# Performance work log

Measured on AMD Instinct MI355X. Metric: run time of the kernel, lower is better.

Reference implementation:

```python
import jax, jax.numpy as jnp
import numpy as np

B, S, D = 32, 1024, 256
F_, K = 256, 3
T = 8192
LN_EPS = 1e-5


def _conv1d(x, w, b, padding):
    # x: [B, S, C_in], w: [C_out, C_in, K] -> [B, S, C_out]
    y = jax.lax.conv_general_dilated(
        x.transpose(0, 2, 1), w, window_strides=(1,),
        padding=[(padding, padding)], dimension_numbers=('NCH', 'OIH', 'NCH'))
    return y.transpose(0, 2, 1) + b


def _layernorm(x, g, b):
    mu = jnp.mean(x, axis=-1, keepdims=True)
    var = jnp.mean(jnp.square(x - mu), axis=-1, keepdims=True)
    return (x - mu) * jax.lax.rsqrt(var + LN_EPS) * g + b


def setup_inputs() -> dict:
    key = jax.random.key(0)
    ks = jax.random.split(key, 8)
    sc = 0.02
    return {
        'x': jax.random.normal(ks[0], (B, S, D), dtype=jnp.float32),
        'mask': jnp.zeros((B, S), dtype=bool),
        'duration': jax.random.randint(ks[1], (B, S), 0, 8, dtype=jnp.int32),
        'max_len': T,
        'conv1_w': jax.random.normal(ks[2], (F_, D, K), dtype=jnp.float32) * sc,
        'conv1_b': jnp.zeros((F_,), dtype=jnp.float32),
        'ln1_g': jnp.ones((F_,), dtype=jnp.float32),
        'ln1_b': jnp.zeros((F_,), dtype=jnp.float32),
        'conv2_w': jax.random.normal(ks[3], (F_, F_, K), dtype=jnp.float32) * sc,
        'conv2_b': jnp.zeros((F_,), dtype=jnp.float32),
        'ln2_g': jnp.ones((F_,), dtype=jnp.float32),
        'ln2_b': jnp.zeros((F_,), dtype=jnp.float32),
        'lin_w': jax.random.normal(ks[4], (F_, 1), dtype=jnp.float32) * sc,
        'lin_b': jnp.zeros((1,), dtype=jnp.float32),
    }


def reference(x, mask, duration, max_len, conv1_w, conv1_b, ln1_g, ln1_b,
              conv2_w, conv2_b, ln2_g, ln2_b, lin_w, lin_b):
    # ---- duration predictor (eval mode: dropout = identity) ----
    h = _conv1d(x, conv1_w, conv1_b, (K - 1) // 2)
    h = _layernorm(jax.nn.relu(h), ln1_g, ln1_b)
    h = _conv1d(h, conv2_w, conv2_b, 1)
    h = _layernorm(jax.nn.relu(h), ln2_g, ln2_b)
    log_dur = (h @ lin_w + lin_b)[..., 0]  # [B, S]
    log_dur = jnp.where(mask, 0.0, log_dur)

    # ---- length regulator: repeat_interleave + pad, done as one gather ----
    dur = duration.astype(jnp.int32)
    cum = jnp.cumsum(dur, axis=1)                                   # [B, S]
    t = jnp.arange(max_len, dtype=jnp.int32)                        # [T]
    src_idx = jax.vmap(lambda c: jnp.searchsorted(c, t, side='right'))(cum)  # [B, T]
    mel_len = jnp.minimum(cum[:, -1], max_len)                      # [B]
    valid = t[None, :] < mel_len[:, None]                           # [B, T]
    src_idx = jnp.clip(src_idx, 0, x.shape[1] - 1)
    out = jnp.take_along_axis(x, src_idx[:, :, None], axis=1)       # [B, T, D]
    out = jnp.where(valid[:, :, None], out, 0.0)
    # duration_target path -> duration_rounded = duration, mel_mask stays None
    return out, log_dur, dur, mel_len
```

## Files before the change

kernel.cpp:

```cpp
#include <hip/hip_runtime.h>
#include <cstddef>

constexpr int Bb   = 32;
constexpr int Ss   = 1024;
constexpr int Dd   = 256;
constexpr int Ff   = 256;
constexpr int TMAX = 8192;
constexpr int MM   = Bb * Ss;
constexpr int KK   = 768;
constexpr int SP   = 1026;
constexpr float LN_EPS = 1e-5f;
constexpr int OPIT = 264;

constexpr int GEMM_BLK  = MM / 64;
constexpr int RIDER_PER = 2048;
constexpr int RIDER_F4  = 4096;

constexpr int PREP_W   = 1536;
constexpr int PREP_X   = Bb * SP * 64 / 256;
constexpr int PREP_CUM = Bb;
constexpr int PREP_PAD = 16;
constexpr int PREP_TOT = PREP_W + PREP_X + PREP_CUM + PREP_PAD;

typedef __bf16 bf16x8 __attribute__((ext_vector_type(8)));
typedef __bf16 bf16x4 __attribute__((ext_vector_type(4)));
typedef float  f32x4  __attribute__((ext_vector_type(4)));

#define GLOAD_LDS16(gp, lp)                                                     \
    __builtin_amdgcn_global_load_lds(                                           \
        (const __attribute__((address_space(1))) void*)(gp),                    \
        (__attribute__((address_space(3))) void*)(lp), 16, 0, 0)

__global__ __launch_bounds__(256) void prep_k(
    const float* __restrict__ w1, const float* __restrict__ w2,
    __bf16* __restrict__ wTTs1, __bf16* __restrict__ wTTs2,
    const float* __restrict__ x, __bf16* __restrict__ xp1,
    const int* __restrict__ dur, float* __restrict__ dur_out,
    float* __restrict__ mel_out, int* __restrict__ idx,
    __bf16* __restrict__ xp2)
{
    __shared__ int ic[1024];
    __shared__ int sc[256];
    const int blk = blockIdx.x;
    const int tid = threadIdx.x;

    if (blk < PREP_W) {
        int i = blk * 256 + tid;
        const float* w = w1;
        __bf16* o = wTTs1;
        int j = i;
        if (j >= Ff * KK) { j -= Ff * KK; w = w2; o = wTTs2; }
        int e   = j & 7;
        int cph = (j >> 3) & 7;
        int r   = (j >> 6) & 255;
        int st  = j >> 14;
        int clog = cph ^ (r & 7);
        int kk  = st * 64 + clog * 8 + e;
        int k   = kk >> 8, d = kk & 255;
        o[j] = (__bf16)w[((size_t)(r * 256 + d)) * 3 + k];
        return;
    }
    if (blk < PREP_W + PREP_X) {
        int i   = (blk - PREP_W) * 256 + tid;
        int row = i >> 6;
        int d4  = (i & 63) * 4;
        int b   = row / SP;
        int j   = row - b * SP;
        bf16x4 o = (bf16x4)(__bf16)0.f;
        if (j != 0 && j != SP - 1) {
            float4 v = *(const float4*)&x[(((size_t)(b << 10) + (j - 1)) << 8) + d4];
            o[0] = (__bf16)v.x; o[1] = (__bf16)v.y;
            o[2] = (__bf16)v.z; o[3] = (__bf16)v.w;
        }
        *(bf16x4*)&xp1[((size_t)row << 8) + d4] = o;
        return;
    }
    if (blk >= PREP_W + PREP_X + PREP_CUM) {
        int j = (blk - (PREP_W + PREP_X + PREP_CUM)) * 256 + tid;
        int b = j >> 7;
        int r = (j >> 6) & 1;
        int d = (j & 63) * 4;
        *(bf16x4*)&xp2[((size_t)b * SP + (size_t)r * (SP - 1)) * 256 + d] =
            (bf16x4)(__bf16)0.f;
        return;
    }
    int b = blk - (PREP_W + PREP_X);
    int4 d4 = ((const int4*)(dur + b * 1024))[tid];
    int l0 = d4.x, l1 = l0 + d4.y, l2 = l1 + d4.z, l3 = l2 + d4.w;
    sc[tid] = l3;
    __syncthreads();
    for (int off = 1; off < 256; off <<= 1) {
        int v = (tid >= off) ? sc[tid - off] : 0;
        __syncthreads();
        sc[tid] += v;
        __syncthreads();
    }
    int excl = sc[tid] - l3;
    ((int4*)ic)[tid] = make_int4(excl + l0, excl + l1, excl + l2, excl + l3);
    ((float4*)(dur_out + b * 1024))[tid] =
        make_float4((float)d4.x, (float)d4.y, (float)d4.z, (float)d4.w);
    if (tid == 255) mel_out[b] = (float)min(excl + l3, TMAX);
    __syncthreads();
    int mel = min(ic[1023], TMAX);
    for (int t = tid; t < TMAX; t += 256) {
        int lo = 0, hi = 1024;
        #pragma unroll
        for (int it = 0; it < 10; ++it) {
            int mid = (lo + hi) >> 1;
            if (ic[mid] <= t) lo = mid + 1; else hi = mid;
        }
        idx[b * TMAX + t] = (t < mel) ? min(lo, 1023) : -1;
    }
}

template<int MODE>
__global__ __launch_bounds__(256, 3) void gemm_fused(
    const float* __restrict__ Xf,
    const __bf16* __restrict__ Ap,
    const __bf16* __restrict__ BwS,
    const float* __restrict__ bias,
    const float* __restrict__ g, const float* __restrict__ bt,
    const float* __restrict__ lw, const float* __restrict__ lb,
    const unsigned char* __restrict__ mask,
    __bf16* __restrict__ outB, float* __restrict__ outF,
    const int* __restrict__ idx, f32x4* __restrict__ outv)
{
    __shared__ __bf16 SMEM[64 * 64 + 256 * 64 + 1088];
    __bf16* As = SMEM;
    __bf16* Bs = SMEM + 4096;

    const int tid = threadIdx.x;

    if (blockIdx.x >= GEMM_BLK) {
        int rblk = blockIdx.x - GEMM_BLK + MODE * RIDER_PER;
        size_t base = (size_t)rblk * RIDER_F4 + tid;
        int sarr[16];
        #pragma unroll
        for (int it = 0; it < 16; ++it) {
            size_t gg = base + (size_t)it * 256;
            sarr[it] = idx[gg >> 6];
        }
        f32x4 v[16];
        #pragma unroll
        for (int it = 0; it < 16; ++it) {
            size_t gg = base + (size_t)it * 256;
            int row = (int)(gg >> 6);
            int col = (int)(gg & 63);
            v[it] = (f32x4)0.f;
            if (sarr[it] >= 0) {
                int b = row >> 13;
                v[it] = ((const f32x4*)Xf)[((size_t)(b << 10) + sarr[it]) * 64 + col];
            }
        }
        #pragma unroll
        for (int it = 0; it < 16; ++it)
            __builtin_nontemporal_store(v[it], &outv[base + (size_t)it * 256]);
        return;
    }

    const int m0   = blockIdx.x * 64;
    const int bb   = m0 >> 10;
    const int s0   = m0 & 1023;
    const int wave = tid >> 6;
    const int lane = tid & 63;
    const int wn   = wave * 64;
    const int lm   = lane & 15;
    const int lk   = lane >> 4;
    const int l3   = lane & 7;
    const int lr   = lane >> 3;

    const int aLaneOff = lr * 256 + ((l3 ^ lr) << 3);
    const int ch0 = lk ^ (lm & 7);

    f32x4 acc[4][4] = {};

    const size_t aRowBase = ((size_t)(bb * SP + s0)) << 8;

    for (int step = 0; step < 12; ++step) {
        const int kk0  = step * 64;
        const int kblk = kk0 >> 8;
        const int d0   = kk0 & 255;

        const __bf16* aSrc = Ap + aRowBase + ((size_t)kblk << 8) + d0 + aLaneOff;
        #pragma unroll
        for (int i = 0; i < 2; ++i) {
            int grp = wave * 2 + i;
            GLOAD_LDS16(aSrc + (size_t)grp * 2048, As + grp * 512);
        }
        const __bf16* bSrc = BwS + (size_t)step * 16384 + lane * 8;
        #pragma unroll
        for (int i = 0; i < 8; ++i) {
            int grp = wave * 8 + i;
            GLOAD_LDS16(bSrc + (size_t)grp * 512, Bs + grp * 512);
        }
        __syncthreads();

        #pragma unroll
        for (int kc = 0; kc < 2; ++kc) {
            const int ch = ch0 ^ (kc << 2);
            bf16x8 af[4], bfr[4];
            #pragma unroll
            for (int mi = 0; mi < 4; ++mi)
                af[mi] = *(const bf16x8*)&As[(mi * 16 + lm) * 64 + ch * 8];
            #pragma unroll
            for (int ni = 0; ni < 4; ++ni)
                bfr[ni] = *(const bf16x8*)&Bs[(wn + ni * 16 + lm) * 64 + ch * 8];
            #pragma unroll
            for (int mi = 0; mi < 4; ++mi)
                #pragma unroll
                for (int ni = 0; ni < 4; ++ni)
                    acc[mi][ni] = __builtin_amdgcn_mfma_f32_16x16x32_bf16(
                        af[mi], bfr[ni], acc[mi][ni], 0, 0, 0);
        }
        __syncthreads();
    }

    float* scrS = (float*)As;
    float* scrQ = scrS + 256;

    float s_[4][4] = {}, q_[4][4] = {};
    #pragma unroll
    for (int ni = 0; ni < 4; ++ni) {
        float bv = bias[wn + ni * 16 + lm];
        #pragma unroll
        for (int mi = 0; mi < 4; ++mi)
            #pragma unroll
            for (int r = 0; r < 4; ++r) {
                float h = fmaxf(acc[mi][ni][r] + bv, 0.f);
                acc[mi][ni][r] = h;
                s_[mi][r] += h;
                q_[mi][r] += h * h;
            }
    }
    #pragma unroll
    for (int off = 1; off < 16; off <<= 1)
        #pragma unroll
        for (int mi = 0; mi < 4; ++mi)
            #pragma unroll
            for (int r = 0; r < 4; ++r) {
                s_[mi][r] += __shfl_xor(s_[mi][r], off, 64);
                q_[mi][r] += __shfl_xor(q_[mi][r], off, 64);
            }
    if (lm == 0) {
        #pragma unroll
        for (int mi = 0; mi < 4; ++mi)
            #pragma unroll
            for (int r = 0; r < 4; ++r) {
                int row = mi * 16 + lk * 4 + r;
                scrS[wave * 64 + row] = s_[mi][r];
                scrQ[wave * 64 + row] = q_[mi][r];
            }
    }
    __syncthreads();

    float mu[4][4], rs[4][4];
    #pragma unroll
    for (int mi = 0; mi < 4; ++mi)
        #pragma unroll
        for (int r = 0; r < 4; ++r) {
            int row = mi * 16 + lk * 4 + r;
            float S = scrS[row] + scrS[64 + row] + scrS[128 + row] + scrS[192 + row];
            float Q = scrQ[row] + scrQ[64 + row] + scrQ[128 + row] + scrQ[192 + row];
            float m_ = S * (1.f / 256.f);
            float v_ = Q * (1.f / 256.f) - m_ * m_;
            mu[mi][r] = m_;
            rs[mi][r] = rsqrtf(v_ + LN_EPS);
        }

    if constexpr (MODE == 0) {
        __bf16* tile = Bs;
        #pragma unroll
        for (int ni = 0; ni < 4; ++ni) {
            int col = wn + ni * 16 + lm;
            float gv = g[col], bv2 = bt[col];
            #pragma unroll
            for (int mi = 0; mi < 4; ++mi)
                #pragma unroll
                for (int r = 0; r < 4; ++r) {
                    int row = mi * 16 + lk * 4 + r;
                    float o = (acc[mi][ni][r] - mu[mi][r]) * rs[mi][r] * gv + bv2;
                    tile[row * OPIT + col] = (__bf16)o;
                }
        }
        __syncthreads();
        size_t obase = ((size_t)(bb * SP + s0 + 1)) << 8;
        #pragma unroll
        for (int i = 0; i < 8; ++i) {
            int c = i * 256 + tid;
            int row = c >> 5, q = c & 31;
            *(bf16x8*)&outB[obase + ((size_t)row << 8) + q * 8] =
                *(bf16x8*)&tile[row * OPIT + q * 8];
        }
    } else {
        float p_[4][4] = {};
        #pragma unroll
        for (int ni = 0; ni < 4; ++ni) {
            int col = wn + ni * 16 + lm;
            float gv = g[col], bv2 = bt[col], wv = lw[col];
            #pragma unroll
            for (int mi = 0; mi < 4; ++mi)
                #pragma unroll
                for (int r = 0; r < 4; ++r) {
                    float o = (acc[mi][ni][r] - mu[mi][r]) * rs[mi][r] * gv + bv2;
                    p_[mi][r] += o * wv;
                }
        }
        #pragma unroll
        for (int off = 1; off < 16; off <<= 1)
            #pragma unroll
            for (int mi = 0; mi < 4; ++mi)
                #pragma unroll
                for (int r = 0; r < 4; ++r)
                    p_[mi][r] += __shfl_xor(p_[mi][r], off, 64);
        __syncthreads();
        if (lm == 0) {
            #pragma unroll
            for (int mi = 0; mi < 4; ++mi)
                #pragma unroll
                for (int r = 0; r < 4; ++r)
                    scrS[wave * 64 + (mi * 16 + lk * 4 + r)] = p_[mi][r];
        }
        __syncthreads();
        if (tid < 64) {
            int row = tid;
            float v = scrS[row] + scrS[64 + row] + scrS[128 + row] + scrS[192 + row]
                      + lb[0];
            if (mask[m0 + row]) v = 0.f;
            outF[m0 + row] = v;
        }
    }
}

extern "C" void kernel_launch(void* const* d_in, const int* in_sizes, int n_in,
                              void* d_out, int out_size, void* d_ws, size_t ws_size,
                              hipStream_t stream)
{
    const float* x            = (const float*)d_in[0];
    const unsigned char* mask = (const unsigned char*)d_in[1];
    const int* duration       = (const int*)d_in[2];
    const float* w1  = (const float*)d_in[4];
    const float* b1  = (const float*)d_in[5];
    const float* g1  = (const float*)d_in[6];
    const float* be1 = (const float*)d_in[7];
    const float* w2  = (const float*)d_in[8];
    const float* b2  = (const float*)d_in[9];
    const float* g2  = (const float*)d_in[10];
    const float* be2 = (const float*)d_in[11];
    const float* lw  = (const float*)d_in[12];
    const float* lb  = (const float*)d_in[13];

    float* out        = (float*)d_out;
    float* out0       = out;
    float* out_logdur = out + (size_t)Bb * TMAX * Dd;
    float* out_dur    = out_logdur + (size_t)Bb * Ss;
    float* out_mel    = out_dur + (size_t)Bb * Ss;

    char* ws = (char*)d_ws;
    __bf16* xp1   = (__bf16*)ws;
    __bf16* xp2   = xp1 + (size_t)Bb * SP * 256;
    __bf16* wTTs1 = xp2 + (size_t)Bb * SP * 256;
    __bf16* wTTs2 = wTTs1 + (size_t)Ff * KK;
    int*    idx   = (int*)(wTTs2 + (size_t)Ff * KK);

    prep_k<<<PREP_TOT, 256, 0, stream>>>(w1, w2, wTTs1, wTTs2, x, xp1,
                                         duration, out_dur, out_mel, idx, xp2);
    gemm_fused<0><<<GEMM_BLK + RIDER_PER, 256, 0, stream>>>(
        x, xp1, wTTs1, b1, g1, be1, nullptr, nullptr, nullptr,
        xp2, nullptr, idx, (f32x4*)out0);
    gemm_fused<1><<<GEMM_BLK + RIDER_PER, 256, 0, stream>>>(
        x, xp2, wTTs2, b2, g2, be2, lw, lb, mask,
        nullptr, out_logdur, idx, (f32x4*)out0);
}
```

Before: 338.4 us.

## Fuse x fp32-to-bf16 conversion into conv1 GEMM and interleave rider blocks

Drops the prep pass that wrote a padded bf16 copy of x; the MODE 0 GEMM now loads fp32 x directly, converts it to bf16 and writes it into swizzled LDS, handling the halo rows inline. Block indices are also interleaved so every fifth block is a GEMM tile and the other four are gather riders, spreading memory-bound gather work alongside compute tiles. This saves a full read and write of x and its bf16 copy, but in exchange conv1 loses the async global_load_lds path and rereads fp32 x (twice the bytes) three times, once per kernel tap.

Result: slower. 383.8 us (+13.4%).

```diff
diff --git a/kernel.cpp b/kernel.cpp
--- a/kernel.cpp
+++ b/kernel.cpp
@@ -15,12 +15,12 @@
 constexpr int GEMM_BLK  = MM / 64;
 constexpr int RIDER_PER = 2048;
 constexpr int RIDER_F4  = 4096;
+constexpr int FUSED_GRID = GEMM_BLK + RIDER_PER;
 
 constexpr int PREP_W   = 1536;
-constexpr int PREP_X   = Bb * SP * 64 / 256;
 constexpr int PREP_CUM = Bb;
 constexpr int PREP_PAD = 16;
-constexpr int PREP_TOT = PREP_W + PREP_X + PREP_CUM + PREP_PAD;
+constexpr int PREP_TOT = PREP_W + PREP_CUM + PREP_PAD;
 
 typedef __bf16 bf16x8 __attribute__((ext_vector_type(8)));
 typedef __bf16 bf16x4 __attribute__((ext_vector_type(4)));
@@ -34,7 +34,6 @@
 __global__ __launch_bounds__(256) void prep_k(
     const float* __restrict__ w1, const float* __restrict__ w2,
     __bf16* __restrict__ wTTs1, __bf16* __restrict__ wTTs2,
-    const float* __restrict__ x, __bf16* __restrict__ xp1,
     const int* __restrict__ dur, float* __restrict__ dur_out,
     float* __restrict__ mel_out, int* __restrict__ idx,
     __bf16* __restrict__ xp2)
@@ -60,23 +59,8 @@
         o[j] = (__bf16)w[((size_t)(r * 256 + d)) * 3 + k];
         return;
     }
-    if (blk < PREP_W + PREP_X) {
-        int i   = (blk - PREP_W) * 256 + tid;
-        int row = i >> 6;
-        int d4  = (i & 63) * 4;
-        int b   = row / SP;
-        int j   = row - b * SP;
-        bf16x4 o = (bf16x4)(__bf16)0.f;
-        if (j != 0 && j != SP - 1) {
-            float4 v = *(const float4*)&x[(((size_t)(b << 10) + (j - 1)) << 8) + d4];
-            o[0] = (__bf16)v.x; o[1] = (__bf16)v.y;
-            o[2] = (__bf16)v.z; o[3] = (__bf16)v.w;
-        }
-        *(bf16x4*)&xp1[((size_t)row << 8) + d4] = o;
-        return;
-    }
-    if (blk >= PREP_W + PREP_X + PREP_CUM) {
-        int j = (blk - (PREP_W + PREP_X + PREP_CUM)) * 256 + tid;
+    if (blk >= PREP_W + PREP_CUM) {
+        int j = (blk - (PREP_W + PREP_CUM)) * 256 + tid;
         int b = j >> 7;
         int r = (j >> 6) & 1;
         int d = (j & 63) * 4;
@@ -84,7 +68,7 @@
             (bf16x4)(__bf16)0.f;
         return;
     }
-    int b = blk - (PREP_W + PREP_X);
+    int b = blk - PREP_W;
     int4 d4 = ((const int4*)(dur + b * 1024))[tid];
     int l0 = d4.x, l1 = l0 + d4.y, l2 = l1 + d4.z, l3 = l2 + d4.w;
     sc[tid] = l3;
@@ -130,9 +114,10 @@
     __bf16* Bs = SMEM + 4096;
 
     const int tid = threadIdx.x;
-
-    if (blockIdx.x >= GEMM_BLK) {
-        int rblk = blockIdx.x - GEMM_BLK + MODE * RIDER_PER;
+    const int gi  = blockIdx.x;
+
+    if (gi % 5 != 0) {
+        int rblk = gi - gi / 5 - 1 + MODE * RIDER_PER;
         size_t base = (size_t)rblk * RIDER_F4 + tid;
         int sarr[16];
         #pragma unroll
@@ -158,7 +143,7 @@
         return;
     }
 
-    const int m0   = blockIdx.x * 64;
+    const int m0   = (gi / 5) * 64;
     const int bb   = m0 >> 10;
     const int s0   = m0 & 1023;
     const int wave = tid >> 6;
@@ -181,11 +166,29 @@
         const int kblk = kk0 >> 8;
         const int d0   = kk0 & 255;
 
-        const __bf16* aSrc = Ap + aRowBase + ((size_t)kblk << 8) + d0 + aLaneOff;
-        #pragma unroll
-        for (int i = 0; i < 2; ++i) {
-            int grp = wave * 2 + i;
-            GLOAD_LDS16(aSrc + (size_t)grp * 2048, As + grp * 512);
+        if constexpr (MODE == 0) {
+            #pragma unroll
+            for (int i = 0; i < 4; ++i) {
+                int c = i * 256 + tid;
+                int r = c >> 4, q = c & 15;
+                int sg = s0 + r + kblk - 1;
+                bf16x4 o = (bf16x4)(__bf16)0.f;
+                if ((unsigned)sg < 1024u) {
+                    float4 v = *(const float4*)&Xf[
+                        (((size_t)(bb << 10) + sg) << 8) + d0 + q * 4];
+                    o[0] = (__bf16)v.x; o[1] = (__bf16)v.y;
+                    o[2] = (__bf16)v.z; o[3] = (__bf16)v.w;
+                }
+                int ch = (q >> 1) ^ (r & 7);
+                *(bf16x4*)&As[r * 64 + ch * 8 + (q & 1) * 4] = o;
+            }
+        } else {
+            const __bf16* aSrc = Ap + aRowBase + ((size_t)kblk << 8) + d0 + aLaneOff;
+            #pragma unroll
+            for (int i = 0; i < 2; ++i) {
+                int grp = wave * 2 + i;
+                GLOAD_LDS16(aSrc + (size_t)grp * 2048, As + grp * 512);
+            }
         }
         const __bf16* bSrc = BwS + (size_t)step * 16384 + lane * 8;
         #pragma unroll
@@ -356,18 +359,17 @@
     float* out_mel    = out_dur + (size_t)Bb * Ss;
 
     char* ws = (char*)d_ws;
-    __bf16* xp1   = (__bf16*)ws;
-    __bf16* xp2   = xp1 + (size_t)Bb * SP * 256;
+    __bf16* xp2   = (__bf16*)ws;
     __bf16* wTTs1 = xp2 + (size_t)Bb * SP * 256;
     __bf16* wTTs2 = wTTs1 + (size_t)Ff * KK;
     int*    idx   = (int*)(wTTs2 + (size_t)Ff * KK);
 
-    prep_k<<<PREP_TOT, 256, 0, stream>>>(w1, w2, wTTs1, wTTs2, x, xp1,
+    prep_k<<<PREP_TOT, 256, 0, stream>>>(w1, w2, wTTs1, wTTs2,
                                          duration, out_dur, out_mel, idx, xp2);
-    gemm_fused<0><<<GEMM_BLK + RIDER_PER, 256, 0, stream>>>(
-        x, xp1, wTTs1, b1, g1, be1, nullptr, nullptr, nullptr,
+    gemm_fused<0><<<FUSED_GRID, 256, 0, stream>>>(
+        x, nullptr, wTTs1, b1, g1, be1, nullptr, nullptr, nullptr,
         xp2, nullptr, idx, (f32x4*)out0);
-    gemm_fused<1><<<GEMM_BLK + RIDER_PER, 256, 0, stream>>>(
+    gemm_fused<1><<<FUSED_GRID, 256, 0, stream>>>(
         x, xp2, wTTs2, b2, g2, be2, lw, lb, mask,
         nullptr, out_logdur, idx, (f32x4*)out0);
 }
```

## Split cumsum into own kernel and spread gather riders across three kernels

Applied to the files above, without the earlier changes.

Moves the duration cumsum and searchsorted into a small separate kernel launched first, so the prep kernel can also carry part of the length-regulator gather. The 4096 gather blocks are now split about evenly across prep and the two GEMM kernels instead of only the two GEMMs. The aim is to balance memory-bound gather work against the compute work and hide it. In exchange it adds one extra kernel launch, and the 32-block cumsum kernel runs serially at low occupancy.

New measurement: 345.1 us. About the same (+2.0%).

```diff
diff --git a/kernel.cpp b/kernel.cpp
--- a/kernel.cpp
+++ b/kernel.cpp
@@ -12,15 +12,17 @@
 constexpr float LN_EPS = 1e-5f;
 constexpr int OPIT = 264;
 
-constexpr int GEMM_BLK  = MM / 64;
-constexpr int RIDER_PER = 2048;
-constexpr int RIDER_F4  = 4096;
-
-constexpr int PREP_W   = 1536;
-constexpr int PREP_X   = Bb * SP * 64 / 256;
-constexpr int PREP_CUM = Bb;
-constexpr int PREP_PAD = 16;
-constexpr int PREP_TOT = PREP_W + PREP_X + PREP_CUM + PREP_PAD;
+constexpr int GEMM_BLK = MM / 64;
+constexpr int RIDER_F4 = 4096;
+constexpr int RID_TOT  = 4096;
+constexpr int RID_PREP = 1366;
+constexpr int RID_F    = 1365;
+
+constexpr int PREP_W    = 1536;
+constexpr int PREP_X    = Bb * SP * 64 / 256;
+constexpr int PREP_PAD  = 16;
+constexpr int PREP_RID0 = PREP_W + PREP_X + PREP_PAD;
+constexpr int PREP_TOT  = PREP_RID0 + RID_PREP;
 
 typedef __bf16 bf16x8 __attribute__((ext_vector_type(8)));
 typedef __bf16 bf16x4 __attribute__((ext_vector_type(4)));
@@ -31,16 +33,76 @@
         (const __attribute__((address_space(1))) void*)(gp),                    \
         (__attribute__((address_space(3))) void*)(lp), 16, 0, 0)
 
+__device__ __forceinline__ void run_rider(
+    int rblk, const float* __restrict__ Xf, const int* __restrict__ idx,
+    f32x4* __restrict__ outv, int tid)
+{
+    size_t base = (size_t)rblk * RIDER_F4 + tid;
+    int sarr[16];
+    #pragma unroll
+    for (int it = 0; it < 16; ++it) {
+        size_t gg = base + (size_t)it * 256;
+        sarr[it] = idx[gg >> 6];
+    }
+    f32x4 v[16];
+    #pragma unroll
+    for (int it = 0; it < 16; ++it) {
+        size_t gg = base + (size_t)it * 256;
+        int row = (int)(gg >> 6);
+        int col = (int)(gg & 63);
+        v[it] = (f32x4)0.f;
+        if (sarr[it] >= 0) {
+            int b = row >> 13;
+            v[it] = ((const f32x4*)Xf)[((size_t)(b << 10) + sarr[it]) * 64 + col];
+        }
+    }
+    #pragma unroll
+    for (int it = 0; it < 16; ++it)
+        __builtin_nontemporal_store(v[it], &outv[base + (size_t)it * 256]);
+}
+
+__global__ __launch_bounds__(256) void cum_k(
+    const int* __restrict__ dur, float* __restrict__ dur_out,
+    float* __restrict__ mel_out, int* __restrict__ idx)
+{
+    __shared__ int ic[1024];
+    __shared__ int sc[256];
+    int b = blockIdx.x, tid = threadIdx.x;
+    int4 d4 = ((const int4*)(dur + b * 1024))[tid];
+    int l0 = d4.x, l1 = l0 + d4.y, l2 = l1 + d4.z, l3 = l2 + d4.w;
+    sc[tid] = l3;
+    __syncthreads();
+    for (int off = 1; off < 256; off <<= 1) {
+        int v = (tid >= off) ? sc[tid - off] : 0;
+        __syncthreads();
+        sc[tid] += v;
+        __syncthreads();
+    }
+    int excl = sc[tid] - l3;
+    ((int4*)ic)[tid] = make_int4(excl + l0, excl + l1, excl + l2, excl + l3);
+    ((float4*)(dur_out + b * 1024))[tid] =
+        make_float4((float)d4.x, (float)d4.y, (float)d4.z, (float)d4.w);
+    if (tid == 255) mel_out[b] = (float)min(excl + l3, TMAX);
+    __syncthreads();
+    int mel = min(ic[1023], TMAX);
+    for (int t = tid; t < TMAX; t += 256) {
+        int lo = 0, hi = 1024;
+        #pragma unroll
+        for (int it = 0; it < 10; ++it) {
+            int mid = (lo + hi) >> 1;
+            if (ic[mid] <= t) lo = mid + 1; else hi = mid;
+        }
+        idx[b * TMAX + t] = (t < mel) ? min(lo, 1023) : -1;
+    }
+}
+
 __global__ __launch_bounds__(256) void prep_k(
     const float* __restrict__ w1, const float* __restrict__ w2,
     __bf16* __restrict__ wTTs1, __bf16* __restrict__ wTTs2,
     const float* __restrict__ x, __bf16* __restrict__ xp1,
-    const int* __restrict__ dur, float* __restrict__ dur_out,
-    float* __restrict__ mel_out, int* __restrict__ idx,
-    __bf16* __restrict__ xp2)
-{
-    __shared__ int ic[1024];
-    __shared__ int sc[256];
+    __bf16* __restrict__ xp2,
+    const int* __restrict__ idx, f32x4* __restrict__ outv)
+{
     const int blk = blockIdx.x;
     const int tid = threadIdx.x;
 
@@ -75,8 +137,8 @@
         *(bf16x4*)&xp1[((size_t)row << 8) + d4] = o;
         return;
     }
-    if (blk >= PREP_W + PREP_X + PREP_CUM) {
-        int j = (blk - (PREP_W + PREP_X + PREP_CUM)) * 256 + tid;
+    if (blk < PREP_RID0) {
+        int j = (blk - (PREP_W + PREP_X)) * 256 + tid;
         int b = j >> 7;
         int r = (j >> 6) & 1;
         int d = (j & 63) * 4;
@@ -84,33 +146,7 @@
             (bf16x4)(__bf16)0.f;
         return;
     }
-    int b = blk - (PREP_W + PREP_X);
-    int4 d4 = ((const int4*)(dur + b * 1024))[tid];
-    int l0 = d4.x, l1 = l0 + d4.y, l2 = l1 + d4.z, l3 = l2 + d4.w;
-    sc[tid] = l3;
-    __syncthreads();
-    for (int off = 1; off < 256; off <<= 1) {
-        int v = (tid >= off) ? sc[tid - off] : 0;
-        __syncthreads();
-        sc[tid] += v;
-        __syncthreads();
-    }
-    int excl = sc[tid] - l3;
-    ((int4*)ic)[tid] = make_int4(excl + l0, excl + l1, excl + l2, excl + l3);
-    ((float4*)(dur_out + b * 1024))[tid] =
-        make_float4((float)d4.x, (float)d4.y, (float)d4.z, (float)d4.w);
-    if (tid == 255) mel_out[b] = (float)min(excl + l3, TMAX);
-    __syncthreads();
-    int mel = min(ic[1023], TMAX);
-    for (int t = tid; t < TMAX; t += 256) {
-        int lo = 0, hi = 1024;
-        #pragma unroll
-        for (int it = 0; it < 10; ++it) {
-            int mid = (lo + hi) >> 1;
-            if (ic[mid] <= t) lo = mid + 1; else hi = mid;
-        }
-        idx[b * TMAX + t] = (t < mel) ? min(lo, 1023) : -1;
-    }
+    run_rider(blk - PREP_RID0, x, idx, outv, tid);
 }
 
 template<int MODE>
@@ -123,7 +159,7 @@
     const float* __restrict__ lw, const float* __restrict__ lb,
     const unsigned char* __restrict__ mask,
     __bf16* __restrict__ outB, float* __restrict__ outF,
-    const int* __restrict__ idx, f32x4* __restrict__ outv)
+    const int* __restrict__ idx, f32x4* __restrict__ outv, int riderBase)
 {
     __shared__ __bf16 SMEM[64 * 64 + 256 * 64 + 1088];
     __bf16* As = SMEM;
@@ -132,29 +168,7 @@
     const int tid = threadIdx.x;
 
     if (blockIdx.x >= GEMM_BLK) {
-        int rblk = blockIdx.x - GEMM_BLK + MODE * RIDER_PER;
-        size_t base = (size_t)rblk * RIDER_F4 + tid;
-        int sarr[16];
-        #pragma unroll
-        for (int it = 0; it < 16; ++it) {
-            size_t gg = base + (size_t)it * 256;
-            sarr[it] = idx[gg >> 6];
-        }
-        f32x4 v[16];
-        #pragma unroll
-        for (int it = 0; it < 16; ++it) {
-            size_t gg = base + (size_t)it * 256;
-            int row = (int)(gg >> 6);
-            int col = (int)(gg & 63);
-            v[it] = (f32x4)0.f;
-            if (sarr[it] >= 0) {
-                int b = row >> 13;
-                v[it] = ((const f32x4*)Xf)[((size_t)(b << 10) + sarr[it]) * 64 + col];
-            }
-        }
-        #pragma unroll
-        for (int it = 0; it < 16; ++it)
-            __builtin_nontemporal_store(v[it], &outv[base + (size_t)it * 256]);
+        run_rider(riderBase + (int)blockIdx.x - GEMM_BLK, Xf, idx, outv, tid);
         return;
     }
 
@@ -362,12 +376,13 @@
     __bf16* wTTs2 = wTTs1 + (size_t)Ff * KK;
     int*    idx   = (int*)(wTTs2 + (size_t)Ff * KK);
 
-    prep_k<<<PREP_TOT, 256, 0, stream>>>(w1, w2, wTTs1, wTTs2, x, xp1,
-                                         duration, out_dur, out_mel, idx, xp2);
-    gemm_fused<0><<<GEMM_BLK + RIDER_PER, 256, 0, stream>>>(
+    cum_k<<<Bb, 256, 0, stream>>>(duration, out_dur, out_mel, idx);
+    prep_k<<<PREP_TOT, 256, 0, stream>>>(w1, w2, wTTs1, wTTs2, x, xp1, xp2,
+                                         idx, (f32x4*)out0);
+    gemm_fused<0><<<GEMM_BLK + RID_F, 256, 0, stream>>>(
         x, xp1, wTTs1, b1, g1, be1, nullptr, nullptr, nullptr,
-        xp2, nullptr, idx, (f32x4*)out0);
-    gemm_fused<1><<<GEMM_BLK + RIDER_PER, 256, 0, stream>>>(
+        xp2, nullptr, idx, (f32x4*)out0, RID_PREP);
+    gemm_fused<1><<<GEMM_BLK + RID_F, 256, 0, stream>>>(
         x, xp2, wTTs2, b2, g2, be2, lw, lb, mask,
-        nullptr, out_logdur, idx, (f32x4*)out0);
-}
+        nullptr, out_logdur, idx, (f32x4*)out0, RID_PREP + RID_F);
+}
```
